# Kernel tuning notes

Hardware: AMD Instinct MI355X
Metric: run time of the kernel (lower is better)

Reference implementation:

```python
import jax, jax.numpy as jnp
import numpy as np
import math

B, S, D, H = 4, 1024, 1024, 16
HD = D // H          # 64
ROT = 32             # min(head_dim, 32)


def _rope(q, k, freqs):
    # q, k: [B,H,S,HD]; freqs: [ROT//2]
    rd = 2 * freqs.shape[0]
    s = q.shape[2]
    pos = jnp.arange(s, dtype=jnp.float32)
    emb = pos[:, None] * freqs[None, :]            # [S, rd/2]
    cos = jnp.cos(emb)[None, None, :, :]           # [1,1,S,rd/2]
    sin = jnp.sin(emb)[None, None, :, :]

    def rot(x):
        xr, xp = x[..., :rd], x[..., rd:]
        xr = xr.reshape(*xr.shape[:-1], rd // 2, 2)
        x0 = xr[..., 0] * cos - xr[..., 1] * sin
        x1 = xr[..., 1] * cos + xr[..., 0] * sin
        xr = jnp.stack([x0, x1], axis=-1).reshape(*x.shape[:-1], rd)
        return jnp.concatenate([xr, xp], axis=-1)

    return rot(q), rot(k)


def setup_inputs() -> dict:
    key = jax.random.key(0)
    ks = jax.random.split(key, 16)
    lin = lambda k: jax.random.normal(k, (D, D), jnp.float32) * 0.02
    inp = {
        'real': jax.random.normal(ks[0], (B, S, D), jnp.float32),
        'imag': jax.random.normal(ks[1], (B, S, D), jnp.float32),
        'attention_mask': jnp.zeros((B, S), dtype=bool),
        'wq_r': lin(ks[2]), 'bq_r': jnp.zeros((D,), jnp.float32),
        'wk_r': lin(ks[3]), 'bk_r': jnp.zeros((D,), jnp.float32),
        'wv_r': lin(ks[4]), 'bv_r': jnp.zeros((D,), jnp.float32),
        'wq_i': lin(ks[5]), 'bq_i': jnp.zeros((D,), jnp.float32),
        'wk_i': lin(ks[6]), 'bk_i': jnp.zeros((D,), jnp.float32),
        'wv_i': lin(ks[7]), 'bv_i': jnp.zeros((D,), jnp.float32),
        'wo_r': lin(ks[8]), 'bo_r': jnp.zeros((D,), jnp.float32),
        'wo_i': lin(ks[9]), 'bo_i': jnp.zeros((D,), jnp.float32),
        'phase_shifts': jax.random.normal(ks[10], (H, HD), jnp.float32) * 0.02,
        'entanglement': jnp.eye(H, dtype=jnp.float32)
                        + jax.random.normal(ks[11], (H, H), jnp.float32) * 0.01,
        'rotary_freqs': (10000.0 ** (-jnp.arange(0, ROT, 2, dtype=jnp.float32) / ROT)),
        'interference_strength': jnp.ones((1,), jnp.float32),
        'attention_temperature': jnp.ones((1,), jnp.float32),
    }
    return inp


def reference(real, imag, attention_mask,
              wq_r, bq_r, wk_r, bk_r, wv_r, bv_r,
              wq_i, bq_i, wk_i, bk_i, wv_i, bv_i,
              wo_r, bo_r, wo_i, bo_i,
              phase_shifts, entanglement, rotary_freqs,
              interference_strength, attention_temperature):
    b, s, d = real.shape
    h, hd = phase_shifts.shape

    def proj(x, w, bias):  # [B,S,D] -> [B,H,S,HD]
        return (x @ w + bias).reshape(b, s, h, hd).transpose(0, 2, 1, 3)

    q_r = proj(real, wq_r, bq_r); k_r = proj(real, wk_r, bk_r); v_r = proj(real, wv_r, bv_r)
    q_i = proj(imag, wq_i, bq_i); k_i = proj(imag, wk_i, bk_i); v_i = proj(imag, wv_i, bv_i)

    q_r, k_r = _rope(q_r, k_r, rotary_freqs)
    q_i, k_i = _rope(q_i, k_i, rotary_freqs)

    # entanglement mixing across heads
    q_r = jnp.einsum('bhsd,hx->bxsd', q_r, entanglement)
    q_i = jnp.einsum('bhsd,hx->bxsd', q_i, entanglement)
    k_r = jnp.einsum('bhsd,hx->bxsd', k_r, entanglement)
    k_i = jnp.einsum('bhsd,hx->bxsd', k_i, entanglement)

    pc = jnp.cos(phase_shifts)[None, :, None, :]   # [1,H,1,HD]
    ps = jnp.sin(phase_shifts)[None, :, None, :]
    qr, qi = q_r * pc - q_i * ps, q_r * ps + q_i * pc
    kr, ki = k_r * pc - k_i * ps, k_r * ps + k_i * pc

    scale = 1.0 / math.sqrt(hd)
    attn_r = (jnp.einsum('bhqd,bhkd->bhqk', qr, kr)
              + jnp.einsum('bhqd,bhkd->bhqk', qi, ki)) * scale
    attn_i = (jnp.einsum('bhqd,bhkd->bhqk', qi, kr)
              - jnp.einsum('bhqd,bhkd->bhqk', qr, ki)) * scale
    attn_mag = jnp.sqrt(attn_r ** 2 + attn_i ** 2 + 1e-6)

    causal = jnp.triu(jnp.ones((s, s), dtype=bool), 1)[None, None]       # [1,1,S,S]
    final_mask = causal | attention_mask[:, None, None, :]               # [B,1,S,S]

    temp = jnp.maximum(attention_temperature, 0.01)
    strength = jax.nn.sigmoid(interference_strength)
    logits = jnp.where(final_mask, -jnp.inf, attn_mag * strength / temp)
    attn_w = jax.nn.softmax(logits, axis=-1)

    out_r = jnp.einsum('bhqk,bhkd->bhqd', attn_w, v_r).transpose(0, 2, 1, 3).reshape(b, s, d)
    out_i = jnp.einsum('bhqk,bhkd->bhqd', attn_w, v_i).transpose(0, 2, 1, 3).reshape(b, s, d)
    out_r = out_r @ wo_r + bo_r
    out_i = out_i @ wo_i + bo_i
    return out_r, out_i
```

## Files before the change

kernel.cpp:

```cpp
#include <hip/hip_runtime.h>
#include <hip/hip_bf16.h>


typedef __attribute__((ext_vector_type(8))) short bf16x8;
typedef __attribute__((ext_vector_type(4))) short bf16x4;
typedef __attribute__((ext_vector_type(4))) float f32x4;

#define DEV static __device__ __forceinline__

DEV short f2b(float f) {
    __hip_bfloat16 h = __float2bfloat16(f);
    short s; __builtin_memcpy(&s, &h, 2); return s;
}
DEV float b2f(short s) {
    unsigned u = ((unsigned)(unsigned short)s) << 16;
    float f; __builtin_memcpy(&f, &u, 4); return f;
}

DEV f32x4 mfma(bf16x8 a, bf16x8 b, f32x4 c) {
    return __builtin_amdgcn_mfma_f32_16x16x32_bf16(a, b, c, 0, 0, 0);
}

DEV void gload16(const void* g, void* l) {
    __builtin_amdgcn_global_load_lds(
        (const __attribute__((address_space(1))) void*)g,
        (__attribute__((address_space(3))) void*)l, 16, 0, 0);
}

DEV void storeC(float* C, size_t idx, float v) { C[idx] = v; }
DEV void storeC(short* C, size_t idx, float v) { C[idx] = f2b(v); }

__global__ __launch_bounds__(256) void k_f2b(const float* __restrict__ in,
                                             short* __restrict__ out) {
    int i = (blockIdx.x * 256 + threadIdx.x) * 4;
    float4 v = *reinterpret_cast<const float4*>(&in[i]);
    bf16x4 o;
    o[0] = f2b(v.x); o[1] = f2b(v.y); o[2] = f2b(v.z); o[3] = f2b(v.w);
    *reinterpret_cast<bf16x4*>(&out[i]) = o;
}

__global__ __launch_bounds__(256) void k_wtrans(
    const float* W0, const float* W1, const float* W2, const float* W3,
    const float* W4, const float* W5, const float* W6, const float* W7,
    short* __restrict__ WtBase) {
    __shared__ short T[64][72];
    int z = blockIdx.z;
    const float* W = z == 0 ? W0 : z == 1 ? W1 : z == 2 ? W2 : z == 3 ? W3
                   : z == 4 ? W4 : z == 5 ? W5 : z == 6 ? W6 : W7;
    short* Wt = WtBase + (size_t)z * 1024 * 1024;
    int n0 = blockIdx.x * 64, k0 = blockIdx.y * 64;
    int t = threadIdx.x;
    for (int i = 0; i < 4; ++i) {
        int idx = t + i * 256; int r = idx >> 4; int c4 = idx & 15;
        float4 v = *reinterpret_cast<const float4*>(&W[(size_t)(k0 + r) * 1024 + n0 + c4 * 4]);
        T[c4 * 4 + 0][r] = f2b(v.x); T[c4 * 4 + 1][r] = f2b(v.y);
        T[c4 * 4 + 2][r] = f2b(v.z); T[c4 * 4 + 3][r] = f2b(v.w);
    }
    __syncthreads();
    for (int i = 0; i < 2; ++i) {
        int idx = t + i * 256; int r = idx >> 3; int c8 = idx & 7;
        bf16x8 v;
        for (int j = 0; j < 8; ++j) v[j] = T[r][c8 * 8 + j];
        *reinterpret_cast<bf16x8*>(&Wt[(size_t)(n0 + r) * 1024 + k0 + c8 * 8]) = v;
    }
}

template <typename OutT>
__global__ __launch_bounds__(256) void k_gemm(
    const short* A0, const short* A1, const short* A2,
    const short* B0, const short* B1, const short* B2,
    const float* b0, const float* b1, const float* b2,
    OutT* C0, OutT* C1, OutT* C2) {
    __shared__ short As[128][32];
    __shared__ short Bs[128][32];
    int z = blockIdx.z;
    const short* A  = z == 0 ? A0 : z == 1 ? A1 : A2;
    const short* BT = z == 0 ? B0 : z == 1 ? B1 : B2;
    const float* bias = z == 0 ? b0 : z == 1 ? b1 : b2;
    OutT* C = z == 0 ? C0 : z == 1 ? C1 : C2;

    int t = threadIdx.x;
    int w = t >> 6, l = t & 63;
    int lr = l & 15, lg = l >> 4;
    int wr = w >> 1, wc = w & 1;
    int row0 = blockIdx.y * 128, col0 = blockIdx.x * 128;

    f32x4 acc[4][4] = {};
    for (int k0 = 0; k0 < 1024; k0 += 32) {
        __syncthreads();
        for (int i = 0; i < 2; ++i) {
            int chunk = i * 256 + t;
            int r = chunk >> 2, c4 = chunk & 3;
            const short* ga = &A[(size_t)(row0 + r) * 1024 + k0 + c4 * 8];
            const short* gb = &BT[(size_t)(col0 + r) * 1024 + k0 + c4 * 8];
            char* la = (char*)&As[0][0] + (size_t)(i * 256 + w * 64) * 16;
            char* lb = (char*)&Bs[0][0] + (size_t)(i * 256 + w * 64) * 16;
            gload16(ga, la);
            gload16(gb, lb);
        }
        __syncthreads();
        bf16x8 af[4], bfr[4];
        for (int m = 0; m < 4; ++m)
            af[m] = *reinterpret_cast<bf16x8*>(&As[wr * 64 + m * 16 + lr][lg * 8]);
        for (int n = 0; n < 4; ++n)
            bfr[n] = *reinterpret_cast<bf16x8*>(&Bs[wc * 64 + n * 16 + lr][lg * 8]);
        for (int m = 0; m < 4; ++m)
            for (int n = 0; n < 4; ++n)
                acc[m][n] = mfma(af[m], bfr[n], acc[m][n]);
    }
    for (int n = 0; n < 4; ++n) {
        int col = col0 + wc * 64 + n * 16 + lr;
        float bv = bias[col];
        for (int m = 0; m < 4; ++m)
            for (int r = 0; r < 4; ++r) {
                int row = row0 + wr * 64 + m * 16 + lg * 4 + r;
                storeC(C, (size_t)row * 1024 + col, acc[m][n][r] + bv);
            }
    }
}

__global__ __launch_bounds__(256) void k_transform(
    const short* __restrict__ Qr, const short* __restrict__ Qi,
    const short* __restrict__ Kr, const short* __restrict__ Ki,
    const float* __restrict__ phase, const float* __restrict__ ent,
    const float* __restrict__ freqs,
    short* __restrict__ oQr, short* __restrict__ oQi,
    short* __restrict__ oKr, short* __restrict__ oKi) {
    __shared__ float xr[1024], xi[1024], E[256];
    int bs = blockIdx.x; int b = bs >> 10; int s = bs & 1023;
    int t = threadIdx.x;
    const short* inR = blockIdx.y ? Kr : Qr;
    const short* inI = blockIdx.y ? Ki : Qi;
    short* outR = blockIdx.y ? oKr : oQr;
    short* outI = blockIdx.y ? oKi : oQi;
    E[t] = ent[t];
    int d0 = t * 4;
    bf16x4 r4 = *reinterpret_cast<const bf16x4*>(&inR[(size_t)bs * 1024 + d0]);
    bf16x4 i4 = *reinterpret_cast<const bf16x4*>(&inI[(size_t)bs * 1024 + d0]);
    float vr[4] = { b2f(r4[0]), b2f(r4[1]), b2f(r4[2]), b2f(r4[3]) };
    float vi[4] = { b2f(i4[0]), b2f(i4[1]), b2f(i4[2]), b2f(i4[3]) };
    if ((d0 & 63) < 32) {
        int p0 = (d0 & 63) >> 1;
        float a0 = (float)s * freqs[p0], a1 = (float)s * freqs[p0 + 1];
        float c0 = cosf(a0), s0 = sinf(a0), c1 = cosf(a1), s1 = sinf(a1);
        float r0, r1;
        r0 = vr[0] * c0 - vr[1] * s0; r1 = vr[1] * c0 + vr[0] * s0; vr[0] = r0; vr[1] = r1;
        r0 = vr[2] * c1 - vr[3] * s1; r1 = vr[3] * c1 + vr[2] * s1; vr[2] = r0; vr[3] = r1;
        r0 = vi[0] * c0 - vi[1] * s0; r1 = vi[1] * c0 + vi[0] * s0; vi[0] = r0; vi[1] = r1;
        r0 = vi[2] * c1 - vi[3] * s1; r1 = vi[3] * c1 + vi[2] * s1; vi[2] = r0; vi[3] = r1;
    }
    for (int j = 0; j < 4; ++j) { xr[d0 + j] = vr[j]; xi[d0 + j] = vi[j]; }
    __syncthreads();
    for (int j = 0; j < 4; ++j) {
        int d = d0 + j; int x = d >> 6; int hd = d & 63;
        float ar = 0.f, ai = 0.f;
        for (int h = 0; h < 16; ++h) {
            float e = E[h * 16 + x];
            ar += xr[h * 64 + hd] * e;
            ai += xi[h * 64 + hd] * e;
        }
        float pc = cosf(phase[d]), ps = sinf(phase[d]);
        float outr = ar * pc - ai * ps;
        float outi = ar * ps + ai * pc;
        size_t oidx = ((size_t)(b * 16 + x) * 1024 + s) * 64 + hd;
        outR[oidx] = f2b(outr);
        outI[oidx] = f2b(outi);
    }
}

__global__ __launch_bounds__(256) void k_vtrans(const short* __restrict__ Vr,
                                                const short* __restrict__ Vi,
                                                short* __restrict__ Vtr,
                                                short* __restrict__ Vti) {
    __shared__ short T[64][72];
    int st = blockIdx.x, h = blockIdx.y, b = blockIdx.z;
    int t = threadIdx.x;
    int s0 = st * 64;
    for (int comp = 0; comp < 2; ++comp) {
        const short* V = comp ? Vi : Vr;
        short* Vt = comp ? Vti : Vtr;
        if (comp) __syncthreads();
        for (int i = 0; i < 2; ++i) {
            int idx = t + i * 256; int r = idx >> 3; int c8 = idx & 7;
            bf16x8 v = *reinterpret_cast<const bf16x8*>(
                &V[(size_t)(b * 1024 + s0 + r) * 1024 + h * 64 + c8 * 8]);
            for (int j = 0; j < 8; ++j) T[c8 * 8 + j][r] = v[j];
        }
        __syncthreads();
        for (int i = 0; i < 2; ++i) {
            int idx = t + i * 256; int r = idx >> 3; int c8 = idx & 7;
            bf16x8 v;
            for (int j = 0; j < 8; ++j) v[j] = T[r][c8 * 8 + j];
            *reinterpret_cast<bf16x8*>(
                &Vt[((size_t)(b * 16 + h) * 64 + r) * 1024 + s0 + c8 * 8]) = v;
        }
    }
}

__global__ __launch_bounds__(256) void k_attn(
    const short* __restrict__ Qr, const short* __restrict__ Qi,
    const short* __restrict__ Kr, const short* __restrict__ Ki,
    const short* __restrict__ Vtr, const short* __restrict__ Vti,
    const float* __restrict__ istr, const float* __restrict__ itemp,
    short* __restrict__ Or, short* __restrict__ Oi) {
    __shared__ short Ks_r[64][72], Ks_i[64][72], Vs_r[64][72], Vs_i[64][72];
    __shared__ short Pl[4][16][72];
    int qt = (int)gridDim.x - 1 - blockIdx.x;
    int h = blockIdx.y, b = blockIdx.z;
    int t = threadIdx.x, w = t >> 6, l = t & 63;
    int lr = l & 15, lg = l >> 4;
    float coef = (1.f / (1.f + __expf(-istr[0]))) / fmaxf(itemp[0], 0.01f);
    const float scale = 0.125f;
    int qrow_a = qt * 64 + w * 16 + lr;
    size_t qbase = ((size_t)(b * 16 + h) * 1024 + qrow_a) * 64;
    bf16x8 fqr[2], fqi[2], fnqr[2];
    for (int kk = 0; kk < 2; ++kk) {
        fqr[kk] = *reinterpret_cast<const bf16x8*>(&Qr[qbase + kk * 32 + lg * 8]);
        fqi[kk] = *reinterpret_cast<const bf16x8*>(&Qi[qbase + kk * 32 + lg * 8]);
        for (int j = 0; j < 8; ++j)
            fnqr[kk][j] = (short)(fqr[kk][j] ^ (short)0x8000);
    }
    f32x4 Oacc_r[4] = {}, Oacc_i[4] = {};
    float m[4], lsum[4];
    for (int r = 0; r < 4; ++r) { m[r] = -__builtin_inff(); lsum[r] = 0.f; }
    size_t kvbase = (size_t)(b * 16 + h) * 1024 * 64;
    int qrow_d = qt * 64 + w * 16 + lg * 4;
    for (int kt = 0; kt <= qt; ++kt) {
        __syncthreads();
        for (int i = 0; i < 2; ++i) {
            int idx = t + i * 256; int r = idx >> 3; int c8 = idx & 7;
            *reinterpret_cast<bf16x8*>(&Ks_r[r][c8 * 8]) =
                *reinterpret_cast<const bf16x8*>(&Kr[kvbase + (size_t)(kt * 64 + r) * 64 + c8 * 8]);
            *reinterpret_cast<bf16x8*>(&Ks_i[r][c8 * 8]) =
                *reinterpret_cast<const bf16x8*>(&Ki[kvbase + (size_t)(kt * 64 + r) * 64 + c8 * 8]);
            *reinterpret_cast<bf16x8*>(&Vs_r[r][c8 * 8]) =
                *reinterpret_cast<const bf16x8*>(&Vtr[kvbase + (size_t)r * 1024 + kt * 64 + c8 * 8]);
            *reinterpret_cast<bf16x8*>(&Vs_i[r][c8 * 8]) =
                *reinterpret_cast<const bf16x8*>(&Vti[kvbase + (size_t)r * 1024 + kt * 64 + c8 * 8]);
        }
        __syncthreads();
        f32x4 sr[4] = {}, si[4] = {};
        for (int cg = 0; cg < 4; ++cg) {
            for (int kk = 0; kk < 2; ++kk) {
                bf16x8 fkr = *reinterpret_cast<bf16x8*>(&Ks_r[cg * 16 + lr][kk * 32 + lg * 8]);
                bf16x8 fki = *reinterpret_cast<bf16x8*>(&Ks_i[cg * 16 + lr][kk * 32 + lg * 8]);
                sr[cg] = mfma(fqr[kk], fkr, sr[cg]);
                sr[cg] = mfma(fqi[kk], fki, sr[cg]);
                si[cg] = mfma(fqi[kk], fkr, si[cg]);
                si[cg] = mfma(fnqr[kk], fki, si[cg]);
            }
        }
        float lgt[4][4];
        for (int cg = 0; cg < 4; ++cg) {
            int kcol = kt * 64 + cg * 16 + lr;
            for (int r = 0; r < 4; ++r) {
                float a_r = sr[cg][r] * scale, a_i = si[cg][r] * scale;
                float mag = sqrtf(a_r * a_r + a_i * a_i + 1e-6f);
                lgt[cg][r] = (kcol <= qrow_d + r) ? mag * coef : -__builtin_inff();
            }
        }
        float alpha[4];
        for (int r = 0; r < 4; ++r) {
            float v = fmaxf(fmaxf(lgt[0][r], lgt[1][r]), fmaxf(lgt[2][r], lgt[3][r]));
            v = fmaxf(v, __shfl_xor(v, 1)); v = fmaxf(v, __shfl_xor(v, 2));
            v = fmaxf(v, __shfl_xor(v, 4)); v = fmaxf(v, __shfl_xor(v, 8));
            float mn = fmaxf(m[r], v);
            alpha[r] = (m[r] == -__builtin_inff()) ? 0.f : __expf(m[r] - mn);
            m[r] = mn;
        }
        float psum[4] = {0.f, 0.f, 0.f, 0.f};
        for (int cg = 0; cg < 4; ++cg)
            for (int r = 0; r < 4; ++r) {
                float p = __expf(lgt[cg][r] - m[r]);
                psum[r] += p;
                Pl[w][lg * 4 + r][cg * 16 + lr] = f2b(p);
            }
        for (int r = 0; r < 4; ++r) {
            float v = psum[r];
            v += __shfl_xor(v, 1); v += __shfl_xor(v, 2);
            v += __shfl_xor(v, 4); v += __shfl_xor(v, 8);
            lsum[r] = lsum[r] * alpha[r] + v;
        }
        __syncthreads();
        for (int cg = 0; cg < 4; ++cg)
            for (int r = 0; r < 4; ++r) { Oacc_r[cg][r] *= alpha[r]; Oacc_i[cg][r] *= alpha[r]; }
        for (int kk = 0; kk < 2; ++kk) {
            bf16x8 fp = *reinterpret_cast<bf16x8*>(&Pl[w][lr][kk * 32 + lg * 8]);
            for (int cg = 0; cg < 4; ++cg) {
                bf16x8 fvr = *reinterpret_cast<bf16x8*>(&Vs_r[cg * 16 + lr][kk * 32 + lg * 8]);
                bf16x8 fvi = *reinterpret_cast<bf16x8*>(&Vs_i[cg * 16 + lr][kk * 32 + lg * 8]);
                Oacc_r[cg] = mfma(fp, fvr, Oacc_r[cg]);
                Oacc_i[cg] = mfma(fp, fvi, Oacc_i[cg]);
            }
        }
    }
    for (int cg = 0; cg < 4; ++cg)
        for (int r = 0; r < 4; ++r) {
            int q = qrow_d + r;
            float inv = 1.f / lsum[r];
            size_t oidx = ((size_t)(b * 1024 + q)) * 1024 + h * 64 + cg * 16 + lr;
            Or[oidx] = f2b(Oacc_r[cg][r] * inv);
            Oi[oidx] = f2b(Oacc_i[cg][r] * inv);
        }
}

extern "C" void kernel_launch(void* const* d_in, const int* in_sizes, int n_in,
                              void* d_out, int out_size, void* d_ws, size_t ws_size,
                              hipStream_t stream) {
    (void)in_sizes; (void)n_in; (void)out_size; (void)ws_size;
    const float* real = (const float*)d_in[0];
    const float* imag = (const float*)d_in[1];
    const float* W[8]    = { (const float*)d_in[3],  (const float*)d_in[5],  (const float*)d_in[7],
                             (const float*)d_in[9],  (const float*)d_in[11], (const float*)d_in[13],
                             (const float*)d_in[15], (const float*)d_in[17] };
    const float* bias[8] = { (const float*)d_in[4],  (const float*)d_in[6],  (const float*)d_in[8],
                             (const float*)d_in[10], (const float*)d_in[12], (const float*)d_in[14],
                             (const float*)d_in[16], (const float*)d_in[18] };
    const float* phase = (const float*)d_in[19];
    const float* ent   = (const float*)d_in[20];
    const float* freqs = (const float*)d_in[21];
    const float* istr  = (const float*)d_in[22];
    const float* itemp = (const float*)d_in[23];
    float* out = (float*)d_out;

    char* p = (char*)d_ws;
    const size_t MB = 1024 * 1024;
    short* Wt  = (short*)(p + 0);
    short* Xr  = (short*)(p + 16 * MB);
    short* Xi  = (short*)(p + 24 * MB);
    short* Qr  = (short*)(p + 32 * MB);
    short* Kr  = (short*)(p + 40 * MB);
    short* Qi  = (short*)(p + 48 * MB);
    short* Ki  = (short*)(p + 56 * MB);
    short* Vr  = (short*)(p + 64 * MB);
    short* Vi  = (short*)(p + 72 * MB);
    short* tQr = (short*)(p + 80 * MB);
    short* tQi = (short*)(p + 88 * MB);
    short* tKr = (short*)(p + 96 * MB);
    short* tKi = (short*)(p + 104 * MB);
    short* Vtr = (short*)(p + 112 * MB);
    short* Vti = (short*)(p + 120 * MB);
    short* Obr = (short*)(p + 128 * MB);
    short* Obi = (short*)(p + 136 * MB);

    dim3 blk(256);
    k_f2b<<<dim3(4096), blk, 0, stream>>>(real, Xr);
    k_f2b<<<dim3(4096), blk, 0, stream>>>(imag, Xi);
    k_wtrans<<<dim3(16, 16, 8), blk, 0, stream>>>(W[0], W[1], W[2], W[3],
                                                  W[4], W[5], W[6], W[7], Wt);
    k_gemm<short><<<dim3(8, 32, 3), blk, 0, stream>>>(
        Xr, Xr, Xr,
        Wt + 0 * MB, Wt + 1 * MB, Wt + 2 * MB,
        bias[0], bias[1], bias[2],
        Qr, Kr, Vr);
    k_gemm<short><<<dim3(8, 32, 3), blk, 0, stream>>>(
        Xi, Xi, Xi,
        Wt + 3 * MB, Wt + 4 * MB, Wt + 5 * MB,
        bias[3], bias[4], bias[5],
        Qi, Ki, Vi);
    k_transform<<<dim3(4096, 2), blk, 0, stream>>>(Qr, Qi, Kr, Ki, phase, ent, freqs,
                                                   tQr, tQi, tKr, tKi);
    k_vtrans<<<dim3(16, 16, 4), blk, 0, stream>>>(Vr, Vi, Vtr, Vti);
    k_attn<<<dim3(16, 16, 4), blk, 0, stream>>>(tQr, tQi, tKr, tKi, Vtr, Vti,
                                                istr, itemp, Obr, Obi);
    k_gemm<float><<<dim3(8, 32, 2), blk, 0, stream>>>(
        Obr, Obi, Obi,
        Wt + 6 * MB, Wt + 7 * MB, Wt + 7 * MB,
        bias[6], bias[7], bias[7],
        out, out + 4 * MB, out + 4 * MB);
}
```

Before: 435.8 us.

## Load K/V fragments directly from global in attention, widen GEMM K tile, merge casts

Result: slower. 586.5 us (+34.6%).

```diff
diff --git a/kernel.cpp b/kernel.cpp
--- a/kernel.cpp
+++ b/kernel.cpp
@@ -30,8 +30,12 @@
 DEV void storeC(float* C, size_t idx, float v) { C[idx] = v; }
 DEV void storeC(short* C, size_t idx, float v) { C[idx] = f2b(v); }
 
-__global__ __launch_bounds__(256) void k_f2b(const float* __restrict__ in,
-                                             short* __restrict__ out) {
+__global__ __launch_bounds__(256) void k_f2b(const float* __restrict__ in0,
+                                             const float* __restrict__ in1,
+                                             short* __restrict__ out0,
+                                             short* __restrict__ out1) {
+    const float* in = blockIdx.y ? in1 : in0;
+    short* out = blockIdx.y ? out1 : out0;
     int i = (blockIdx.x * 256 + threadIdx.x) * 4;
     float4 v = *reinterpret_cast<const float4*>(&in[i]);
     bf16x4 o;
@@ -71,8 +75,8 @@
     const short* B0, const short* B1, const short* B2,
     const float* b0, const float* b1, const float* b2,
     OutT* C0, OutT* C1, OutT* C2) {
-    __shared__ short As[128][32];
-    __shared__ short Bs[128][32];
+    __shared__ short As[128][64];
+    __shared__ short Bs[128][64];
     int z = blockIdx.z;
     const short* A  = z == 0 ? A0 : z == 1 ? A1 : A2;
     const short* BT = z == 0 ? B0 : z == 1 ? B1 : B2;
@@ -86,27 +90,27 @@
     int row0 = blockIdx.y * 128, col0 = blockIdx.x * 128;
 
     f32x4 acc[4][4] = {};
-    for (int k0 = 0; k0 < 1024; k0 += 32) {
+    for (int k0 = 0; k0 < 1024; k0 += 64) {
         __syncthreads();
-        for (int i = 0; i < 2; ++i) {
+        for (int i = 0; i < 4; ++i) {
             int chunk = i * 256 + t;
-            int r = chunk >> 2, c4 = chunk & 3;
-            const short* ga = &A[(size_t)(row0 + r) * 1024 + k0 + c4 * 8];
-            const short* gb = &BT[(size_t)(col0 + r) * 1024 + k0 + c4 * 8];
+            int r = chunk >> 3, j = chunk & 7;
             char* la = (char*)&As[0][0] + (size_t)(i * 256 + w * 64) * 16;
             char* lb = (char*)&Bs[0][0] + (size_t)(i * 256 + w * 64) * 16;
-            gload16(ga, la);
-            gload16(gb, lb);
+            gload16(&A[(size_t)(row0 + r) * 1024 + k0 + j * 8], la);
+            gload16(&BT[(size_t)(col0 + r) * 1024 + k0 + j * 8], lb);
         }
         __syncthreads();
-        bf16x8 af[4], bfr[4];
-        for (int m = 0; m < 4; ++m)
-            af[m] = *reinterpret_cast<bf16x8*>(&As[wr * 64 + m * 16 + lr][lg * 8]);
-        for (int n = 0; n < 4; ++n)
-            bfr[n] = *reinterpret_cast<bf16x8*>(&Bs[wc * 64 + n * 16 + lr][lg * 8]);
-        for (int m = 0; m < 4; ++m)
+        for (int kk = 0; kk < 2; ++kk) {
+            bf16x8 af[4], bfr[4];
+            for (int m = 0; m < 4; ++m)
+                af[m] = *reinterpret_cast<bf16x8*>(&As[wr * 64 + m * 16 + lr][kk * 32 + lg * 8]);
             for (int n = 0; n < 4; ++n)
-                acc[m][n] = mfma(af[m], bfr[n], acc[m][n]);
+                bfr[n] = *reinterpret_cast<bf16x8*>(&Bs[wc * 64 + n * 16 + lr][kk * 32 + lg * 8]);
+            for (int m = 0; m < 4; ++m)
+                for (int n = 0; n < 4; ++n)
+                    acc[m][n] = mfma(af[m], bfr[n], acc[m][n]);
+        }
     }
     for (int n = 0; n < 4; ++n) {
         int col = col0 + wc * 64 + n * 16 + lr;
@@ -203,14 +207,14 @@
     const short* __restrict__ Vtr, const short* __restrict__ Vti,
     const float* __restrict__ istr, const float* __restrict__ itemp,
     short* __restrict__ Or, short* __restrict__ Oi) {
-    __shared__ short Ks_r[64][72], Ks_i[64][72], Vs_r[64][72], Vs_i[64][72];
     __shared__ short Pl[4][16][72];
     int qt = (int)gridDim.x - 1 - blockIdx.x;
     int h = blockIdx.y, b = blockIdx.z;
     int t = threadIdx.x, w = t >> 6, l = t & 63;
     int lr = l & 15, lg = l >> 4;
-    float coef = (1.f / (1.f + __expf(-istr[0]))) / fmaxf(itemp[0], 0.01f);
     const float scale = 0.125f;
+    float cs = (1.f / (1.f + __expf(-istr[0]))) / fmaxf(itemp[0], 0.01f) * scale;
+    const float eps2 = 1e-6f / (0.125f * 0.125f);
     int qrow_a = qt * 64 + w * 16 + lr;
     size_t qbase = ((size_t)(b * 16 + h) * 1024 + qrow_a) * 64;
     bf16x8 fqr[2], fqi[2], fnqr[2];
@@ -221,42 +225,35 @@
             fnqr[kk][j] = (short)(fqr[kk][j] ^ (short)0x8000);
     }
     f32x4 Oacc_r[4] = {}, Oacc_i[4] = {};
-    float m[4], lsum[4];
-    for (int r = 0; r < 4; ++r) { m[r] = -__builtin_inff(); lsum[r] = 0.f; }
+    float m[4] = {0.f, 0.f, 0.f, 0.f}, lsum[4] = {0.f, 0.f, 0.f, 0.f};
     size_t kvbase = (size_t)(b * 16 + h) * 1024 * 64;
     int qrow_d = qt * 64 + w * 16 + lg * 4;
     for (int kt = 0; kt <= qt; ++kt) {
-        __syncthreads();
-        for (int i = 0; i < 2; ++i) {
-            int idx = t + i * 256; int r = idx >> 3; int c8 = idx & 7;
-            *reinterpret_cast<bf16x8*>(&Ks_r[r][c8 * 8]) =
-                *reinterpret_cast<const bf16x8*>(&Kr[kvbase + (size_t)(kt * 64 + r) * 64 + c8 * 8]);
-            *reinterpret_cast<bf16x8*>(&Ks_i[r][c8 * 8]) =
-                *reinterpret_cast<const bf16x8*>(&Ki[kvbase + (size_t)(kt * 64 + r) * 64 + c8 * 8]);
-            *reinterpret_cast<bf16x8*>(&Vs_r[r][c8 * 8]) =
-                *reinterpret_cast<const bf16x8*>(&Vtr[kvbase + (size_t)r * 1024 + kt * 64 + c8 * 8]);
-            *reinterpret_cast<bf16x8*>(&Vs_i[r][c8 * 8]) =
-                *reinterpret_cast<const bf16x8*>(&Vti[kvbase + (size_t)r * 1024 + kt * 64 + c8 * 8]);
-        }
-        __syncthreads();
+        const short* Kr_t = Kr + kvbase + (size_t)kt * 64 * 64;
+        const short* Ki_t = Ki + kvbase + (size_t)kt * 64 * 64;
         f32x4 sr[4] = {}, si[4] = {};
         for (int cg = 0; cg < 4; ++cg) {
+            int koff = (cg * 16 + lr) * 64 + lg * 8;
             for (int kk = 0; kk < 2; ++kk) {
-                bf16x8 fkr = *reinterpret_cast<bf16x8*>(&Ks_r[cg * 16 + lr][kk * 32 + lg * 8]);
-                bf16x8 fki = *reinterpret_cast<bf16x8*>(&Ks_i[cg * 16 + lr][kk * 32 + lg * 8]);
+                bf16x8 fkr = *reinterpret_cast<const bf16x8*>(&Kr_t[koff + kk * 32]);
+                bf16x8 fki = *reinterpret_cast<const bf16x8*>(&Ki_t[koff + kk * 32]);
+                __builtin_amdgcn_s_setprio(1);
                 sr[cg] = mfma(fqr[kk], fkr, sr[cg]);
                 sr[cg] = mfma(fqi[kk], fki, sr[cg]);
                 si[cg] = mfma(fqi[kk], fkr, si[cg]);
                 si[cg] = mfma(fnqr[kk], fki, si[cg]);
+                __builtin_amdgcn_s_setprio(0);
             }
         }
         float lgt[4][4];
-        for (int cg = 0; cg < 4; ++cg) {
-            int kcol = kt * 64 + cg * 16 + lr;
-            for (int r = 0; r < 4; ++r) {
-                float a_r = sr[cg][r] * scale, a_i = si[cg][r] * scale;
-                float mag = sqrtf(a_r * a_r + a_i * a_i + 1e-6f);
-                lgt[cg][r] = (kcol <= qrow_d + r) ? mag * coef : -__builtin_inff();
+        for (int cg = 0; cg < 4; ++cg)
+            for (int r = 0; r < 4; ++r)
+                lgt[cg][r] = cs * sqrtf(sr[cg][r] * sr[cg][r] + si[cg][r] * si[cg][r] + eps2);
+        if (kt == qt) {
+            for (int cg = 0; cg < 4; ++cg) {
+                int kcol = kt * 64 + cg * 16 + lr;
+                for (int r = 0; r < 4; ++r)
+                    if (kcol > qrow_d + r) lgt[cg][r] = -__builtin_inff();
             }
         }
         float alpha[4];
@@ -265,7 +262,7 @@
             v = fmaxf(v, __shfl_xor(v, 1)); v = fmaxf(v, __shfl_xor(v, 2));
             v = fmaxf(v, __shfl_xor(v, 4)); v = fmaxf(v, __shfl_xor(v, 8));
             float mn = fmaxf(m[r], v);
-            alpha[r] = (m[r] == -__builtin_inff()) ? 0.f : __expf(m[r] - mn);
+            alpha[r] = __expf(m[r] - mn);
             m[r] = mn;
         }
         float psum[4] = {0.f, 0.f, 0.f, 0.f};
@@ -281,16 +278,21 @@
             v += __shfl_xor(v, 4); v += __shfl_xor(v, 8);
             lsum[r] = lsum[r] * alpha[r] + v;
         }
-        __syncthreads();
         for (int cg = 0; cg < 4; ++cg)
             for (int r = 0; r < 4; ++r) { Oacc_r[cg][r] *= alpha[r]; Oacc_i[cg][r] *= alpha[r]; }
+        const short* Vr_t = Vtr + kvbase + kt * 64;
+        const short* Vi_t = Vti + kvbase + kt * 64;
         for (int kk = 0; kk < 2; ++kk) {
             bf16x8 fp = *reinterpret_cast<bf16x8*>(&Pl[w][lr][kk * 32 + lg * 8]);
             for (int cg = 0; cg < 4; ++cg) {
-                bf16x8 fvr = *reinterpret_cast<bf16x8*>(&Vs_r[cg * 16 + lr][kk * 32 + lg * 8]);
-                bf16x8 fvi = *reinterpret_cast<bf16x8*>(&Vs_i[cg * 16 + lr][kk * 32 + lg * 8]);
+                bf16x8 fvr = *reinterpret_cast<const bf16x8*>(
+                    &Vr_t[(size_t)(cg * 16 + lr) * 1024 + kk * 32 + lg * 8]);
+                bf16x8 fvi = *reinterpret_cast<const bf16x8*>(
+                    &Vi_t[(size_t)(cg * 16 + lr) * 1024 + kk * 32 + lg * 8]);
+                __builtin_amdgcn_s_setprio(1);
                 Oacc_r[cg] = mfma(fp, fvr, Oacc_r[cg]);
                 Oacc_i[cg] = mfma(fp, fvi, Oacc_i[cg]);
+                __builtin_amdgcn_s_setprio(0);
             }
         }
     }
@@ -344,8 +346,7 @@
     short* Obi = (short*)(p + 136 * MB);
 
     dim3 blk(256);
-    k_f2b<<<dim3(4096), blk, 0, stream>>>(real, Xr);
-    k_f2b<<<dim3(4096), blk, 0, stream>>>(imag, Xi);
+    k_f2b<<<dim3(4096, 2), blk, 0, stream>>>(real, imag, Xr, Xi);
     k_wtrans<<<dim3(16, 16, 8), blk, 0, stream>>>(W[0], W[1], W[2], W[3],
                                                   W[4], W[5], W[6], W[7], Wt);
     k_gemm<short><<<dim3(8, 32, 3), blk, 0, stream>>>(
```
